# Optimization experiments

Hardware: AMD Instinct MI355X
Metric: run time of the kernel (lower is better)

## Reference

```python
import jax, jax.numpy as jnp
import numpy as np

NUM_HEADS = 4
KEY_DIM = 8
WINDOW = 4
SHIFT = 2
CHANNELS = 32


def setup_inputs() -> dict:
    key = jax.random.key(0)
    ks = jax.random.split(key, 9)
    C, H, D = CHANNELS, NUM_HEADS, KEY_DIM
    s = 0.05
    return {
        "x": jax.random.normal(ks[0], (4, 512, 512, C), jnp.float32),
        "Wq": jax.random.normal(ks[1], (C, H, D), jnp.float32) * s,
        "bq": jax.random.normal(ks[2], (H, D), jnp.float32) * s,
        "Wk": jax.random.normal(ks[3], (C, H, D), jnp.float32) * s,
        "bk": jax.random.normal(ks[4], (H, D), jnp.float32) * s,
        "Wv": jax.random.normal(ks[5], (C, H, D), jnp.float32) * s,
        "bv": jax.random.normal(ks[6], (H, D), jnp.float32) * s,
        "Wo": jax.random.normal(ks[7], (H, D, C), jnp.float32) * s,
        "bo": jax.random.normal(ks[8], (C,), jnp.float32) * s,
    }


def reference(x, Wq, bq, Wk, bk, Wv, bv, Wo, bo):
    B, H, W, C = x.shape
    ws, sh = WINDOW, SHIFT
    pad_h = (ws - H % ws) % ws
    pad_w = (ws - W % ws) % ws
    p = jnp.pad(x, ((0, 0), (0, pad_h), (0, pad_w), (0, 0)))
    if sh:
        p = jnp.roll(p, shift=(-sh, -sh), axis=(1, 2))
    Hp, Wp = H + pad_h, W + pad_w
    hw, ww = Hp // ws, Wp // ws
    # partition into windows: [B*hw*ww, ws*ws, C]
    win = p.reshape(B, hw, ws, ww, ws, C).transpose(0, 1, 3, 2, 4, 5)
    win = win.reshape(-1, ws * ws, C)
    # multi-head self-attention within each window (Keras MultiHeadAttention math)
    q = jnp.einsum('bnc,chd->bnhd', win, Wq) + bq
    k = jnp.einsum('bnc,chd->bnhd', win, Wk) + bk
    v = jnp.einsum('bnc,chd->bnhd', win, Wv) + bv
    scores = jnp.einsum('bqhd,bkhd->bhqk', q, k) / np.sqrt(KEY_DIM).astype(np.float32)
    attn = jax.nn.softmax(scores, axis=-1)
    o = jnp.einsum('bhqk,bkhd->bqhd', attn, v)
    out = jnp.einsum('bqhd,hdc->bqc', o, Wo) + bo
    # merge windows back: [B, Hp, Wp, C]
    out = out.reshape(B, hw, ww, ws, ws, C).transpose(0, 1, 3, 2, 4, 5)
    out = out.reshape(B, Hp, Wp, C)
    if sh:
        out = jnp.roll(out, shift=(sh, sh), axis=(1, 2))
    out = out[:, :H, :W, :]
    return x + out
```

## Files before the change

### kernel.cpp

```cpp
#include <hip/hip_runtime.h>
#include <hip/hip_bf16.h>
#include <stdint.h>

typedef float f32x4 __attribute__((ext_vector_type(4)));
typedef short s16x8 __attribute__((ext_vector_type(8)));
typedef unsigned short u16;
typedef u16 u16x4 __attribute__((ext_vector_type(4)));

__device__ __forceinline__ u16 f2bf(float f) {
    union { __hip_bfloat16 h; u16 u; } cv;
    cv.h = __float2bfloat16(f);
    return cv.u;
}
__device__ __forceinline__ int pkbf(float lo, float hi) {
    return (int)(unsigned)f2bf(lo) | ((int)(unsigned)f2bf(hi) << 16);
}
__device__ __forceinline__ f32x4 mfma16(s16x8 a, s16x8 b, f32x4 c) {
    return __builtin_amdgcn_mfma_f32_16x16x32_bf16(a, b, c, 0, 0, 0);
}
__device__ __forceinline__ float exp2_hw(float x) {
    float r; asm("v_exp_f32 %0, %1" : "=v"(r) : "v"(x)); return r;
}
__device__ __forceinline__ int swz16(int v) {
    return __builtin_amdgcn_ds_swizzle(v, 0x401F);
}
__device__ __forceinline__ int pl_lo_to_hi(int v) {
    auto r = __builtin_amdgcn_permlane32_swap(v, v, false, false);
    return r[0];
}
__device__ __forceinline__ float xor32_other(float v, bool lo32) {
    auto r = __builtin_amdgcn_permlane32_swap(__float_as_int(v), __float_as_int(v), false, false);
    return lo32 ? __int_as_float(r[1]) : __int_as_float(r[0]);
}
__device__ __forceinline__ s16x8 frag4(int d0, int d1, int d2, int d3) {
    union { int i[4]; s16x8 v; } u;
    u.i[0] = d0; u.i[1] = d1; u.i[2] = d2; u.i[3] = d3;
    return u.v;
}
#define C_FENCE() asm volatile("" ::: "memory")

__global__ __launch_bounds__(256) void swin_attn_kernel(
    const float* __restrict__ x,
    const float* __restrict__ Wq, const float* __restrict__ bq,
    const float* __restrict__ Wk, const float* __restrict__ bk,
    const float* __restrict__ Wv, const float* __restrict__ bv,
    const float* __restrict__ Wo, const float* __restrict__ bo,
    float* __restrict__ out)
{
    const int lane  = threadIdx.x & 63;
    const int wave  = threadIdx.x >> 6;
    const int c16   = lane & 15;
    const int g     = lane >> 4;
    const bool lo32 = (lane < 32);

    __shared__ __align__(16) u16 qk_bf[4][16][72];
    __shared__ __align__(16) u16 vT_bf[4][32][24];
    __shared__ __align__(16) u16 p_bf[4][16][24];

    const float qscale = 0.35355339059327373f * 1.4426950408889634f;

    s16x8 wqkv[6];
    #pragma unroll
    for (int j = 0; j < 6; ++j) {
        const float* Wsrc = (j < 2) ? Wq : (j < 4) ? Wk : Wv;
        const int colW = ((j & 1) << 4) | c16;
        const float sc = (j < 2) ? qscale : 1.0f;
        s16x8 wf;
        #pragma unroll
        for (int jj = 0; jj < 8; ++jj)
            wf[jj] = (short)f2bf(Wsrc[(g * 8 + jj) * 32 + colW] * sc);
        wqkv[j] = wf;
    }
    f32x4 bias_qk[4];
    #pragma unroll
    for (int j = 0; j < 4; ++j) {
        const float* bsrc = (j < 2) ? bq : bk;
        const float sc = (j < 2) ? qscale : 1.0f;
        #pragma unroll
        for (int i = 0; i < 4; ++i)
            bias_qk[j][i] = bsrc[((j & 1) << 4) + 4 * g + i] * sc;
    }
    f32x4 bias_v[2];
    #pragma unroll
    for (int jv = 0; jv < 2; ++jv) {
        float b = bv[jv * 16 + c16];
        bias_v[jv] = (f32x4){b, b, b, b};
    }
    s16x8 wo_frag[2];
    f32x4 bo_frag[2];
    #pragma unroll
    for (int j2 = 0; j2 < 2; ++j2) {
        const int cout = j2 * 16 + c16;
        s16x8 wf;
        #pragma unroll
        for (int jj = 0; jj < 8; ++jj) {
            const int h = (g >> 1) * 2 + (jj >> 2);
            const int d = 4 * (g & 1) + (jj & 3);
            wf[jj] = (short)f2bf(Wo[(h * 8 + d) * 32 + cout]);
        }
        wo_frag[j2] = wf;
        #pragma unroll
        for (int i = 0; i < 4; ++i)
            bo_frag[j2][i] = bo[j2 * 16 + 4 * g + i];
    }

    const f32x4 zero4 = {0.f, 0.f, 0.f, 0.f};
    const s16x8 zero8 = {0, 0, 0, 0, 0, 0, 0, 0};

    const int wbase = (blockIdx.x * 4 + wave) * 4;
    long curpix;
    f32x4 px0, px1;
    {
        const int w = wbase;
        const int b = w >> 14, rem = w & 16383, wi = rem >> 7, wj = rem & 127;
        const int row  = (wi * 4 + (c16 >> 2) + 2) & 511;
        const int colp = (wj * 4 + (c16 & 3) + 2) & 511;
        curpix = ((((long)b << 9) + row) * 512 + colp) * 32;
        px0 = *(const f32x4*)(x + curpix + g * 8);
        px1 = *(const f32x4*)(x + curpix + g * 8 + 4);
    }

    #pragma unroll 1
    for (int it = 0; it < 4; ++it) {
        const long pixbase = curpix;
        s16x8 xfrag = frag4(pkbf(px0[0], px0[1]), pkbf(px0[2], px0[3]),
                            pkbf(px1[0], px1[1]), pkbf(px1[2], px1[3]));

        #pragma unroll
        for (int j = 0; j < 4; ++j) {
            f32x4 c = mfma16(wqkv[j], xfrag, bias_qk[j]);
            u16x4 qv;
            #pragma unroll
            for (int i = 0; i < 4; ++i) qv[i] = f2bf(c[i]);
            *(u16x4*)&qk_bf[wave][c16][j * 16 + 4 * g] = qv;
        }
        #pragma unroll
        for (int jv = 0; jv < 2; ++jv) {
            f32x4 c = mfma16(xfrag, wqkv[4 + jv], bias_v[jv]);
            u16x4 vv;
            #pragma unroll
            for (int i = 0; i < 4; ++i) vv[i] = f2bf(c[i]);
            *(u16x4*)&vT_bf[wave][jv * 16 + c16][4 * g] = vv;
        }

        {
            const int w = wbase + ((it + 1) & 3);
            const int b = w >> 14, rem = w & 16383, wi = rem >> 7, wj = rem & 127;
            const int row  = (wi * 4 + (c16 >> 2) + 2) & 511;
            const int colp = (wj * 4 + (c16 & 3) + 2) & 511;
            const long np = ((((long)b << 9) + row) * 512 + colp) * 32;
            px0 = *(const f32x4*)(x + np + g * 8);
            px1 = *(const f32x4*)(x + np + g * 8 + 4);
            curpix = np;
        }
        f32x4 r0 = *(const f32x4*)(x + pixbase + 4 * g);
        f32x4 r1 = *(const f32x4*)(x + pixbase + 16 + 4 * g);

        C_FENCE();

        f32x4 o_acc[4];
        #pragma unroll
        for (int h = 0; h < 4; ++h) {
            s16x8 afrag = zero8, bfrag = zero8;
            if (g == 0) {
                afrag = *(const s16x8*)&qk_bf[wave][c16][32 + h * 8];
                bfrag = *(const s16x8*)&qk_bf[wave][c16][h * 8];
            }
            f32x4 s = mfma16(afrag, bfrag, zero4);

            float e0 = exp2_hw(s[0]), e1 = exp2_hw(s[1]);
            float e2 = exp2_hw(s[2]), e3 = exp2_hw(s[3]);
            float part = (e0 + e1) + (e2 + e3);
            float sum  = part + __int_as_float(swz16(__float_as_int(part)));
            sum += xor32_other(sum, lo32);
            const float inv = __builtin_amdgcn_rcpf(sum);
            u16x4 pv;
            pv[0] = f2bf(e0 * inv); pv[1] = f2bf(e1 * inv);
            pv[2] = f2bf(e2 * inv); pv[3] = f2bf(e3 * inv);
            *(u16x4*)&p_bf[wave][c16][4 * g] = pv;
            C_FENCE();

            s16x8 vfrag = zero8, pfrag = zero8;
            if (g < 2) {
                vfrag = *(const s16x8*)&vT_bf[wave][h * 8 + (c16 & 7)][g * 8];
                pfrag = *(const s16x8*)&p_bf[wave][c16][g * 8];
            }
            o_acc[h] = mfma16(vfrag, pfrag, zero4);
            C_FENCE();
        }

        int t00 = pkbf(o_acc[0][0], o_acc[0][1]), t01 = pkbf(o_acc[0][2], o_acc[0][3]);
        int t10 = pkbf(o_acc[1][0], o_acc[1][1]), t11 = pkbf(o_acc[1][2], o_acc[1][3]);
        int t20 = pkbf(o_acc[2][0], o_acc[2][1]), t21 = pkbf(o_acc[2][2], o_acc[2][3]);
        int t30 = pkbf(o_acc[3][0], o_acc[3][1]), t31 = pkbf(o_acc[3][2], o_acc[3][3]);
        int m20 = pl_lo_to_hi(t20), m21 = pl_lo_to_hi(t21);
        int m30 = pl_lo_to_hi(t30), m31 = pl_lo_to_hi(t31);
        s16x8 ofrag = frag4(lo32 ? t00 : m20, lo32 ? t01 : m21,
                            lo32 ? t10 : m30, lo32 ? t11 : m31);

        f32x4 ci0 = bo_frag[0], ci1 = bo_frag[1];
        #pragma unroll
        for (int i = 0; i < 4; ++i) { ci0[i] += r0[i]; ci1[i] += r1[i]; }
        f32x4 c0 = mfma16(wo_frag[0], ofrag, ci0);
        f32x4 c1 = mfma16(wo_frag[1], ofrag, ci1);
        *(f32x4*)(out + pixbase + 4 * g) = c0;
        *(f32x4*)(out + pixbase + 16 + 4 * g) = c1;

        C_FENCE();
    }
}

extern "C" void kernel_launch(void* const* d_in, const int* in_sizes, int n_in,
                              void* d_out, int out_size, void* d_ws, size_t ws_size,
                              hipStream_t stream) {
    const float* x  = (const float*)d_in[0];
    const float* Wq = (const float*)d_in[1];
    const float* bq = (const float*)d_in[2];
    const float* Wk = (const float*)d_in[3];
    const float* bk = (const float*)d_in[4];
    const float* Wv = (const float*)d_in[5];
    const float* bv = (const float*)d_in[6];
    const float* Wo = (const float*)d_in[7];
    const float* bo = (const float*)d_in[8];
    float* out = (float*)d_out;

    dim3 grid(4096), block(256);
    hipLaunchKernelGGL(swin_attn_kernel, grid, block, 0, stream,
                       x, Wq, bq, Wk, bk, Wv, bv, Wo, bo, out);
}
```

Measured before the change: 66.90 us.

## Shuffle softmax probabilities in registers and double-buffer LDS across windows

Removes the LDS round-trip for the softmax probability matrix. The probabilities are now rearranged into the MFMA B-fragment with ds_swizzle and permlane32 swaps instead of being stored and reloaded. The Q/K and V LDS staging buffers are double-buffered by iteration parity, and the compiler memory fences are removed so successive windows can overlap. Each wave now processes 8 windows with half the grid, which amortizes per-block weight loading but gives less parallelism and relies on implicit intra-wave LDS ordering without fences.

```diff
diff --git a/kernel.cpp b/kernel.cpp
--- a/kernel.cpp
+++ b/kernel.cpp
@@ -24,20 +24,19 @@
 __device__ __forceinline__ int swz16(int v) {
     return __builtin_amdgcn_ds_swizzle(v, 0x401F);
 }
+__device__ __forceinline__ int xor32i(int v, bool lo32) {
+    auto r = __builtin_amdgcn_permlane32_swap(v, v, false, false);
+    return lo32 ? r[1] : r[0];
+}
 __device__ __forceinline__ int pl_lo_to_hi(int v) {
     auto r = __builtin_amdgcn_permlane32_swap(v, v, false, false);
     return r[0];
-}
-__device__ __forceinline__ float xor32_other(float v, bool lo32) {
-    auto r = __builtin_amdgcn_permlane32_swap(__float_as_int(v), __float_as_int(v), false, false);
-    return lo32 ? __int_as_float(r[1]) : __int_as_float(r[0]);
 }
 __device__ __forceinline__ s16x8 frag4(int d0, int d1, int d2, int d3) {
     union { int i[4]; s16x8 v; } u;
     u.i[0] = d0; u.i[1] = d1; u.i[2] = d2; u.i[3] = d3;
     return u.v;
 }
-#define C_FENCE() asm volatile("" ::: "memory")
 
 __global__ __launch_bounds__(256) void swin_attn_kernel(
     const float* __restrict__ x,
@@ -53,9 +52,8 @@
     const int g     = lane >> 4;
     const bool lo32 = (lane < 32);
 
-    __shared__ __align__(16) u16 qk_bf[4][16][72];
-    __shared__ __align__(16) u16 vT_bf[4][32][24];
-    __shared__ __align__(16) u16 p_bf[4][16][24];
+    __shared__ __align__(16) u16 qk_bf[2][4][16][72];
+    __shared__ __align__(16) u16 vT_bf[2][4][32][24];
 
     const float qscale = 0.35355339059327373f * 1.4426950408889634f;
 
@@ -107,7 +105,7 @@
     const f32x4 zero4 = {0.f, 0.f, 0.f, 0.f};
     const s16x8 zero8 = {0, 0, 0, 0, 0, 0, 0, 0};
 
-    const int wbase = (blockIdx.x * 4 + wave) * 4;
+    const int wbase = (blockIdx.x * 4 + wave) * 8;
     long curpix;
     f32x4 px0, px1;
     {
@@ -120,8 +118,9 @@
         px1 = *(const f32x4*)(x + curpix + g * 8 + 4);
     }
 
-    #pragma unroll 1
-    for (int it = 0; it < 4; ++it) {
+    #pragma unroll 2
+    for (int it = 0; it < 8; ++it) {
+        const int pb = it & 1;
         const long pixbase = curpix;
         s16x8 xfrag = frag4(pkbf(px0[0], px0[1]), pkbf(px0[2], px0[3]),
                             pkbf(px1[0], px1[1]), pkbf(px1[2], px1[3]));
@@ -132,7 +131,7 @@
             u16x4 qv;
             #pragma unroll
             for (int i = 0; i < 4; ++i) qv[i] = f2bf(c[i]);
-            *(u16x4*)&qk_bf[wave][c16][j * 16 + 4 * g] = qv;
+            *(u16x4*)&qk_bf[pb][wave][c16][j * 16 + 4 * g] = qv;
         }
         #pragma unroll
         for (int jv = 0; jv < 2; ++jv) {
@@ -140,11 +139,11 @@
             u16x4 vv;
             #pragma unroll
             for (int i = 0; i < 4; ++i) vv[i] = f2bf(c[i]);
-            *(u16x4*)&vT_bf[wave][jv * 16 + c16][4 * g] = vv;
+            *(u16x4*)&vT_bf[pb][wave][jv * 16 + c16][4 * g] = vv;
         }
 
         {
-            const int w = wbase + ((it + 1) & 3);
+            const int w = wbase + ((it + 1) & 7);
             const int b = w >> 14, rem = w & 16383, wi = rem >> 7, wj = rem & 127;
             const int row  = (wi * 4 + (c16 >> 2) + 2) & 511;
             const int colp = (wj * 4 + (c16 & 3) + 2) & 511;
@@ -156,15 +155,13 @@
         f32x4 r0 = *(const f32x4*)(x + pixbase + 4 * g);
         f32x4 r1 = *(const f32x4*)(x + pixbase + 16 + 4 * g);
 
-        C_FENCE();
-
         f32x4 o_acc[4];
         #pragma unroll
         for (int h = 0; h < 4; ++h) {
             s16x8 afrag = zero8, bfrag = zero8;
             if (g == 0) {
-                afrag = *(const s16x8*)&qk_bf[wave][c16][32 + h * 8];
-                bfrag = *(const s16x8*)&qk_bf[wave][c16][h * 8];
+                afrag = *(const s16x8*)&qk_bf[pb][wave][c16][32 + h * 8];
+                bfrag = *(const s16x8*)&qk_bf[pb][wave][c16][h * 8];
             }
             f32x4 s = mfma16(afrag, bfrag, zero4);
 
@@ -172,21 +169,24 @@
             float e2 = exp2_hw(s[2]), e3 = exp2_hw(s[3]);
             float part = (e0 + e1) + (e2 + e3);
             float sum  = part + __int_as_float(swz16(__float_as_int(part)));
-            sum += xor32_other(sum, lo32);
+            sum += __int_as_float(xor32i(__float_as_int(sum), lo32));
             const float inv = __builtin_amdgcn_rcpf(sum);
-            u16x4 pv;
-            pv[0] = f2bf(e0 * inv); pv[1] = f2bf(e1 * inv);
-            pv[2] = f2bf(e2 * inv); pv[3] = f2bf(e3 * inv);
-            *(u16x4*)&p_bf[wave][c16][4 * g] = pv;
-            C_FENCE();
-
-            s16x8 vfrag = zero8, pfrag = zero8;
-            if (g < 2) {
-                vfrag = *(const s16x8*)&vT_bf[wave][h * 8 + (c16 & 7)][g * 8];
-                pfrag = *(const s16x8*)&p_bf[wave][c16][g * 8];
-            }
+
+            int dwA = pkbf(e0 * inv, e1 * inv);
+            int dwB = pkbf(e2 * inv, e3 * inv);
+            int sA = swz16(dwA), sB = swz16(dwB);
+            int tA = xor32i(dwA, lo32), tB = xor32i(dwB, lo32);
+            int uA = xor32i(sA, lo32),  uB = xor32i(sB, lo32);
+            const bool g0 = (g == 0), g1 = (g == 1);
+            s16x8 pfrag = frag4(g0 ? dwA : (g1 ? uA : 0),
+                                g0 ? dwB : (g1 ? uB : 0),
+                                g0 ? sA  : (g1 ? tA : 0),
+                                g0 ? sB  : (g1 ? tB : 0));
+
+            s16x8 vfrag = zero8;
+            if (g < 2)
+                vfrag = *(const s16x8*)&vT_bf[pb][wave][h * 8 + (c16 & 7)][g * 8];
             o_acc[h] = mfma16(vfrag, pfrag, zero4);
-            C_FENCE();
         }
 
         int t00 = pkbf(o_acc[0][0], o_acc[0][1]), t01 = pkbf(o_acc[0][2], o_acc[0][3]);
@@ -205,8 +205,6 @@
         f32x4 c1 = mfma16(wo_frag[1], ofrag, ci1);
         *(f32x4*)(out + pixbase + 4 * g) = c0;
         *(f32x4*)(out + pixbase + 16 + 4 * g) = c1;
-
-        C_FENCE();
     }
 }
 
@@ -224,7 +222,7 @@
     const float* bo = (const float*)d_in[8];
     float* out = (float*)d_out;
 
-    dim3 grid(4096), block(256);
+    dim3 grid(2048), block(256);
     hipLaunchKernelGGL(swin_attn_kernel, grid, block, 0, stream,
                        x, Wq, bq, Wk, bk, Wv, bv, Wo, bo, out);
 }
```

Result: no change. 68.13 us (+1.8%).
